# Performance work log

Hardware: AMD Instinct MI355X
Metric: run time of the kernel (lower is better)

## Reference

```python
import jax, jax.numpy as jnp
import numpy as np

ACT_BW = 8
PAR_BW = 4
EPS = 1e-8

def fake_quant(t, bw):
    # symmetric per-tensor fake quantization with dynamic absmax observer
    qmax = float(2 ** (bw - 1) - 1)
    scale = jnp.maximum(jnp.max(jnp.abs(t)) / qmax, EPS)
    q = jnp.clip(jnp.round(t / scale), -qmax, qmax) * scale
    # straight-through estimator (matches torch fake-quant backward)
    return t + jax.lax.stop_gradient(q - t)

def setup_inputs() -> dict:
    key = jax.random.key(0)
    k1, k2, k3 = jax.random.split(key, 3)
    tokens, d_in, d_out = 4096, 4096, 4096
    x = jax.random.normal(k1, (tokens, d_in), dtype=jnp.float32)
    # kaiming-uniform-ish init scale
    bound_w = 1.0 / np.sqrt(d_in)
    weight = jax.random.uniform(k2, (d_out, d_in), dtype=jnp.float32, minval=-bound_w, maxval=bound_w)
    b = jax.random.uniform(k3, (d_out,), dtype=jnp.float32, minval=-bound_w, maxval=bound_w)
    return {"x": x, "weight": weight, "b": b}

def reference(x, weight, b):
    # 1) requantize input activations (act_bitwidth)
    xq = fake_quant(x, ACT_BW)
    # 2) quantize weight (par_bitwidth), transpose [out,in] -> [in,out]
    wq = fake_quant(weight, PAR_BW).T
    # 3) quantize bias (act_bitwidth)
    bq = fake_quant(b, ACT_BW)
    # 4) AddMM: bias + x @ w^T, then requantize the output (multiplier's quantizer)
    out = bq + jnp.matmul(xq, wq)  # [tokens, out_features]
    return fake_quant(out, ACT_BW)
```

## Files before the change

kernel.cpp:

```cpp
#include <hip/hip_runtime.h>

#define NELEM (4096 * 4096)
#define KDIM 4096
#define NDIM 4096
#define DOUT 4096
#define EPSQ 1e-8f
#define STRIDE_MEM (2048 * 256)

typedef __attribute__((ext_vector_type(4))) int i32x4;
typedef __attribute__((ext_vector_type(16))) int i32x16;

typedef __attribute__((address_space(3))) void lds_void;
typedef const __attribute__((address_space(1))) void gbl_void;

__device__ __forceinline__ void load_lds16(const void* g, void* l) {
    __builtin_amdgcn_global_load_lds((gbl_void*)g, (lds_void*)l, 16, 0, 0);
}

__device__ __forceinline__ float wave_max64(float v) {
#pragma unroll
    for (int off = 32; off > 0; off >>= 1)
        v = fmaxf(v, __shfl_down(v, off));
    return v;
}


__global__ __launch_bounds__(256) void absmax_xwb(
    const float4* __restrict__ x, const float4* __restrict__ w,
    const float* __restrict__ b, unsigned* __restrict__ amax)
{
    float mx = 0.f, mw = 0.f;
    int i = blockIdx.x * 256 + threadIdx.x;
#pragma unroll
    for (int it = 0; it < 8; ++it, i += STRIDE_MEM) {
        float4 a = x[i];
        float4 c = w[i];
        mx = fmaxf(mx, fmaxf(fmaxf(fabsf(a.x), fabsf(a.y)), fmaxf(fabsf(a.z), fabsf(a.w))));
        mw = fmaxf(mw, fmaxf(fmaxf(fabsf(c.x), fabsf(c.y)), fmaxf(fabsf(c.z), fabsf(c.w))));
    }
    float mb = 0.f;
    if (blockIdx.x == 0) {
#pragma unroll
        for (int t = 0; t < DOUT / 256; ++t)
            mb = fmaxf(mb, fabsf(b[t * 256 + threadIdx.x]));
    }

    mx = wave_max64(mx); mw = wave_max64(mw); mb = wave_max64(mb);
    __shared__ float red[3][4];
    const int wave = threadIdx.x >> 6, lane = threadIdx.x & 63;
    if (lane == 0) { red[0][wave] = mx; red[1][wave] = mw; red[2][wave] = mb; }
    __syncthreads();
    if (threadIdx.x == 0) {
        float r0 = fmaxf(fmaxf(red[0][0], red[0][1]), fmaxf(red[0][2], red[0][3]));
        float r1 = fmaxf(fmaxf(red[1][0], red[1][1]), fmaxf(red[1][2], red[1][3]));
        const int sl = (blockIdx.x & 7) * 16;
        atomicMax(&amax[sl], __float_as_uint(r0));
        atomicMax(&amax[sl + 4], __float_as_uint(r1));
        if (blockIdx.x == 0) {
            float r2 = fmaxf(fmaxf(red[2][0], red[2][1]), fmaxf(red[2][2], red[2][3]));
            atomicMax(&amax[128], __float_as_uint(r2));
        }
    }
}

__device__ __forceinline__ void load_scales(const unsigned* __restrict__ amax,
                                            float& sx, float& sw) {
    float sxm = 0.f, swm = 0.f;
#pragma unroll
    for (int j = 0; j < 8; ++j) {
        sxm = fmaxf(sxm, __uint_as_float(amax[j * 16]));
        swm = fmaxf(swm, __uint_as_float(amax[j * 16 + 4]));
    }
    sx = fmaxf(sxm / 127.0f, EPSQ);
    sw = fmaxf(swm / 7.0f, EPSQ);
}

__device__ __forceinline__ int pack4(float4 a, float s, float qmax) {
    int b0 = (int)fminf(fmaxf(rintf(a.x / s), -qmax), qmax);
    int b1 = (int)fminf(fmaxf(rintf(a.y / s), -qmax), qmax);
    int b2 = (int)fminf(fmaxf(rintf(a.z / s), -qmax), qmax);
    int b3 = (int)fminf(fmaxf(rintf(a.w / s), -qmax), qmax);
    return (b0 & 0xff) | ((b1 & 0xff) << 8) | ((b2 & 0xff) << 16) | (b3 << 24);
}

__global__ __launch_bounds__(256) void quant_xwb(
    const float4* __restrict__ x, const float4* __restrict__ w,
    const float* __restrict__ b, const unsigned* __restrict__ amax,
    int* __restrict__ qx, int* __restrict__ qw, float* __restrict__ bq)
{
    float sx, sw;
    load_scales(amax, sx, sw);
    int i = blockIdx.x * 256 + threadIdx.x;
#pragma unroll
    for (int it = 0; it < 8; ++it, i += STRIDE_MEM) {
        qx[i] = pack4(x[i], sx, 127.f);
        qw[i] = pack4(w[i], sw, 7.f);
    }
    if (blockIdx.x == 0) {
        const float sb = fmaxf(__uint_as_float(amax[128]) / 127.0f, EPSQ);
#pragma unroll
        for (int t = 0; t < DOUT / 256; ++t) {
            int j = t * 256 + threadIdx.x;
            float q = fminf(fmaxf(rintf(b[j] / sb), -127.f), 127.f);
            bq[j] = q * sb;
        }
    }
}

__global__ __launch_bounds__(512, 2) void gemm_i8_8p(
    const char* __restrict__ qx,
    const char* __restrict__ qw,
    const float* __restrict__ bq,
    const unsigned* __restrict__ amax,
    float* __restrict__ out,
    unsigned* __restrict__ amax_out)
{
    constexpr int K = KDIM, N = NDIM;
    __shared__ char lds[131072];
    char* ldsA = lds;
    char* ldsB = lds + 65536;

    const int tid = threadIdx.x;
    const int wave = tid >> 6, lane = tid & 63;
    const int swz = (blockIdx.x & 7) * 32 + (blockIdx.x >> 3);
    const int bm = swz >> 4, bn = swz & 15;
    const int wm2 = wave >> 2;
    const int wn4 = wave & 3;

    const int sg16 = (((lane & 3) ^ ((lane >> 3) & 3)) << 4);
    const char* aG = qx + (size_t)(bm * 256 + wave * 16 + (lane >> 2)) * K + sg16;
    const char* bG = qw + (size_t)(bn * 256 + wave * 16 + (lane >> 2)) * K + sg16;

    const int l31 = lane & 31;
    const int fks0 = ((((lane >> 5)) ^ ((lane >> 1) & 3)) << 4);
    const int fks1 = ((((lane >> 5) | 2) ^ ((lane >> 1) & 3)) << 4);
    const int aBase = wm2 * 8192 + l31 * 64;
    const int bBase = (wn4 >> 1) * 8192 + (wn4 & 1) * 4096 + l31 * 64;

    i32x16 acc[4][2] = {};
    i32x4 XA[4], XB[2], YA[4], YB[2], A1[4], B1[2];

#define STAGE8(s) { const int p_ = (s) & 3;                                                  \
    load_lds16(aG + (size_t)(s) * 64,                   ldsA + p_ * 16384 + wave * 1024);    \
    load_lds16(aG + (size_t)128 * K + (size_t)(s) * 64, ldsA + p_ * 16384 + 8192 + wave * 1024); \
    load_lds16(bG + (size_t)(s) * 64,                   ldsB + p_ * 16384 + wave * 1024);    \
    load_lds16(bG + (size_t)128 * K + (size_t)(s) * 64, ldsB + p_ * 16384 + 8192 + wave * 1024); }

#define PHASE(s, CA, CB, NA, NB, VMN, DO_ST, DO_NXT) {                                       \
    asm volatile("s_waitcnt vmcnt(%0)" :: "n"(VMN) : "memory");                              \
    __builtin_amdgcn_s_barrier();                                                            \
    __builtin_amdgcn_sched_barrier(0);                                                       \
    if (DO_ST) STAGE8((s) + 3);                                                              \
    { const char* Ab_ = ldsA + ((s) & 3) * 16384 + aBase;                                    \
      const char* Bb_ = ldsB + ((s) & 3) * 16384 + bBase;                                    \
      _Pragma("unroll") for (int mi = 0; mi < 4; ++mi)                                       \
          A1[mi] = *(const i32x4*)(Ab_ + mi * 2048 + fks1);                                  \
      _Pragma("unroll") for (int ni = 0; ni < 2; ++ni)                                       \
          B1[ni] = *(const i32x4*)(Bb_ + ni * 2048 + fks1);                                  \
    }                                                                                        \
    __builtin_amdgcn_sched_barrier(0);                                                       \
    __builtin_amdgcn_s_setprio(1);                                                           \
    _Pragma("unroll") for (int mi = 0; mi < 4; ++mi)                                         \
    _Pragma("unroll") for (int ni = 0; ni < 2; ++ni)                                         \
        acc[mi][ni] = __builtin_amdgcn_mfma_i32_32x32x32_i8(CA[mi], CB[ni], acc[mi][ni], 0, 0, 0); \
    __builtin_amdgcn_s_setprio(0);                                                           \
    __builtin_amdgcn_sched_barrier(0);                                                       \
    if (DO_NXT) {                                                                            \
      const char* An_ = ldsA + (((s) + 1) & 3) * 16384 + aBase;                              \
      const char* Bn_ = ldsB + (((s) + 1) & 3) * 16384 + bBase;                              \
      _Pragma("unroll") for (int mi = 0; mi < 4; ++mi)                                       \
          NA[mi] = *(const i32x4*)(An_ + mi * 2048 + fks0);                                  \
      _Pragma("unroll") for (int ni = 0; ni < 2; ++ni)                                       \
          NB[ni] = *(const i32x4*)(Bn_ + ni * 2048 + fks0);                                  \
    }                                                                                        \
    __builtin_amdgcn_sched_barrier(0);                                                       \
    __builtin_amdgcn_s_setprio(1);                                                           \
    _Pragma("unroll") for (int mi = 0; mi < 4; ++mi)                                         \
    _Pragma("unroll") for (int ni = 0; ni < 2; ++ni)                                         \
        acc[mi][ni] = __builtin_amdgcn_mfma_i32_32x32x32_i8(A1[mi], B1[ni], acc[mi][ni], 0, 0, 0); \
    __builtin_amdgcn_s_setprio(0); }

    STAGE8(0); STAGE8(1); STAGE8(2);
    asm volatile("s_waitcnt vmcnt(8)" ::: "memory");
    __builtin_amdgcn_s_barrier();
    __builtin_amdgcn_sched_barrier(0);
    {
        const char* Ab_ = ldsA + aBase;
        const char* Bb_ = ldsB + bBase;
#pragma unroll
        for (int mi = 0; mi < 4; ++mi) XA[mi] = *(const i32x4*)(Ab_ + mi * 2048 + fks0);
#pragma unroll
        for (int ni = 0; ni < 2; ++ni) XB[ni] = *(const i32x4*)(Bb_ + ni * 2048 + fks0);
    }

    for (int s = 0; s < 60; s += 2) {
        PHASE(s,     XA, XB, YA, YB, 4, true, true);
        PHASE(s + 1, YA, YB, XA, XB, 4, true, true);
    }
    PHASE(60, XA, XB, YA, YB, 4, true,  true);
    PHASE(61, YA, YB, XA, XB, 4, false, true);
    PHASE(62, XA, XB, YA, YB, 0, false, true);
    PHASE(63, YA, YB, XA, XB, 0, false, false);

#undef PHASE
#undef STAGE8

    float sx, sw;
    load_scales(amax, sx, sw);
    const float s = sx * sw;
    const int col = l31;
    const int r4 = (lane >> 5) * 4;
    float am = 0.f;
    float bqv[2];
#pragma unroll
    for (int ni = 0; ni < 2; ++ni) bqv[ni] = bq[bn * 256 + wn4 * 64 + ni * 32 + col];

#pragma unroll
    for (int mi = 0; mi < 4; ++mi) {
#pragma unroll
        for (int reg = 0; reg < 16; ++reg) {
            const int row = (reg & 3) + 8 * (reg >> 2) + r4;
            const int m = bm * 256 + wm2 * 128 + mi * 32 + row;
            float* orow = out + (size_t)m * N + bn * 256 + wn4 * 64 + col;
#pragma unroll
            for (int ni = 0; ni < 2; ++ni) {
                float o = fmaf(s, (float)acc[mi][ni][reg], bqv[ni]);
                am = fmaxf(am, fabsf(o));
                orow[ni * 32] = o;
            }
        }
    }
    am = wave_max64(am);
    float* red = (float*)lds;
    if (lane == 0) red[wave] = am;
    __syncthreads();
    if (tid == 0) {
        float r = fmaxf(fmaxf(fmaxf(red[0], red[1]), fmaxf(red[2], red[3])),
                        fmaxf(fmaxf(red[4], red[5]), fmaxf(red[6], red[7])));
        atomicMax(amax_out, __float_as_uint(r));
    }
}

__global__ __launch_bounds__(256) void final_quant(
    float4* __restrict__ out, const unsigned* __restrict__ amax_out)
{
    const float so = fmaxf(__uint_as_float(amax_out[0]) / 127.0f, EPSQ);
    int i = blockIdx.x * 256 + threadIdx.x;
#pragma unroll
    for (int it = 0; it < 8; ++it, i += STRIDE_MEM) {
        float4 v = out[i];
        v.x = fminf(fmaxf(rintf(v.x / so), -127.f), 127.f) * so;
        v.y = fminf(fmaxf(rintf(v.y / so), -127.f), 127.f) * so;
        v.z = fminf(fmaxf(rintf(v.z / so), -127.f), 127.f) * so;
        v.w = fminf(fmaxf(rintf(v.w / so), -127.f), 127.f) * so;
        out[i] = v;
    }
}

extern "C" void kernel_launch(void* const* d_in, const int* in_sizes, int n_in,
                              void* d_out, int out_size, void* d_ws, size_t ws_size,
                              hipStream_t stream) {
    const float* x = (const float*)d_in[0];
    const float* w = (const float*)d_in[1];
    const float* b = (const float*)d_in[2];
    float* out = (float*)d_out;

    char* ws = (char*)d_ws;
    unsigned* amax = (unsigned*)ws;
    float* bq = (float*)(ws + 1024);
    char* qx = (char*)(ws + 32768);
    char* qw = (char*)(ws + 32768 + (size_t)NELEM);

    hipMemsetAsync(amax, 0, 1024, stream);
    hipLaunchKernelGGL(absmax_xwb, dim3(2048), dim3(256), 0, stream,
                       (const float4*)x, (const float4*)w, b, amax);
    hipLaunchKernelGGL(quant_xwb, dim3(2048), dim3(256), 0, stream,
                       (const float4*)x, (const float4*)w, b, amax,
                       (int*)qx, (int*)qw, bq);
    hipLaunchKernelGGL(gemm_i8_8p, dim3(256), dim3(512), 0, stream,
                       (const char*)qx, (const char*)qw, bq, amax, out, amax + 132);
    hipLaunchKernelGGL(final_quant, dim3(2048), dim3(256), 0, stream,
                       (float4*)out, amax + 132);
}
```

Baseline: 278.1 us.

## Fuse output requantization into GEMM epilogue via grid-wide absmax barrier

The GEMM epilogue first computes each block's output absmax and publishes it with an atomic. All blocks then spin on a completion counter until the global max is known, and each block quantizes its own outputs before storing them. This removes the separate read-modify-write pass over the 64MB output in final_quant, which now exits early when a flag shows the fused path succeeded. The spin relies on all 256 blocks being co-resident and falls back through a timeout flag. The LDS swizzle pattern is also changed to add a wave/lane XOR term, aimed at reducing bank conflicts.

```diff
diff --git a/kernel.cpp b/kernel.cpp
--- a/kernel.cpp
+++ b/kernel.cpp
@@ -113,7 +113,7 @@
     const float* __restrict__ bq,
     const unsigned* __restrict__ amax,
     float* __restrict__ out,
-    unsigned* __restrict__ amax_out)
+    unsigned* __restrict__ ws)
 {
     constexpr int K = KDIM, N = NDIM;
     __shared__ char lds[131072];
@@ -127,13 +127,14 @@
     const int wm2 = wave >> 2;
     const int wn4 = wave & 3;
 
-    const int sg16 = (((lane & 3) ^ ((lane >> 3) & 3)) << 4);
+    const int sg16 = (((lane & 3) ^ ((lane >> 3) & 3) ^ (wave & 1)) << 4);
     const char* aG = qx + (size_t)(bm * 256 + wave * 16 + (lane >> 2)) * K + sg16;
     const char* bG = qw + (size_t)(bn * 256 + wave * 16 + (lane >> 2)) * K + sg16;
 
     const int l31 = lane & 31;
-    const int fks0 = ((((lane >> 5)) ^ ((lane >> 1) & 3)) << 4);
-    const int fks1 = ((((lane >> 5) | 2) ^ ((lane >> 1) & 3)) << 4);
+    const int fx = ((lane >> 1) & 3) ^ ((lane >> 4) & 1);
+    const int fks0 = (((lane >> 5) ^ fx) << 4);
+    const int fks1 = ((((lane >> 5) | 2) ^ fx) << 4);
     const int aBase = wm2 * 8192 + l31 * 64;
     const int bBase = (wn4 >> 1) * 8192 + (wn4 & 1) * 4096 + l31 * 64;
 
@@ -216,6 +217,52 @@
     for (int ni = 0; ni < 2; ++ni) bqv[ni] = bq[bn * 256 + wn4 * 64 + ni * 32 + col];
 
 #pragma unroll
+    for (int mi = 0; mi < 4; ++mi)
+#pragma unroll
+        for (int reg = 0; reg < 16; ++reg)
+#pragma unroll
+            for (int ni = 0; ni < 2; ++ni) {
+                float o = fmaf(s, (float)acc[mi][ni][reg], bqv[ni]);
+                am = fmaxf(am, fabsf(o));
+            }
+    am = wave_max64(am);
+    float* red = (float*)lds;
+    if (lane == 0) red[wave] = am;
+    __syncthreads();
+
+    unsigned* amax_out = ws + 132;
+    unsigned* done = ws + 136;
+    unsigned* flag = ws + 140;
+    if (tid == 0) {
+        float r = fmaxf(fmaxf(fmaxf(red[0], red[1]), fmaxf(red[2], red[3])),
+                        fmaxf(fmaxf(red[4], red[5]), fmaxf(red[6], red[7])));
+        atomicMax(amax_out, __float_as_uint(r));
+        __threadfence();
+        unsigned old = atomicAdd(done, 1u);
+        float so = -1.f;
+        if (old == 255u) {
+            __threadfence();
+            atomicOr(flag, 1u);
+            so = fmaxf(__uint_as_float(atomicMax(amax_out, 0u)) / 127.0f, EPSQ);
+        } else {
+            int iters = 0;
+            while (__hip_atomic_load(done, __ATOMIC_RELAXED, __HIP_MEMORY_SCOPE_AGENT) < 256u) {
+                __builtin_amdgcn_s_sleep(2);
+                if (++iters > 150000) break;
+            }
+            if (iters > 150000) {
+                atomicOr(flag, 2u);
+            } else {
+                __threadfence();
+                so = fmaxf(__uint_as_float(atomicMax(amax_out, 0u)) / 127.0f, EPSQ);
+            }
+        }
+        red[12] = so;
+    }
+    __syncthreads();
+    const float so = red[12];
+
+#pragma unroll
     for (int mi = 0; mi < 4; ++mi) {
 #pragma unroll
         for (int reg = 0; reg < 16; ++reg) {
@@ -225,26 +272,19 @@
 #pragma unroll
             for (int ni = 0; ni < 2; ++ni) {
                 float o = fmaf(s, (float)acc[mi][ni][reg], bqv[ni]);
-                am = fmaxf(am, fabsf(o));
+                if (so > 0.f)
+                    o = fminf(fmaxf(rintf(o / so), -127.f), 127.f) * so;
                 orow[ni * 32] = o;
             }
         }
     }
-    am = wave_max64(am);
-    float* red = (float*)lds;
-    if (lane == 0) red[wave] = am;
-    __syncthreads();
-    if (tid == 0) {
-        float r = fmaxf(fmaxf(fmaxf(red[0], red[1]), fmaxf(red[2], red[3])),
-                        fmaxf(fmaxf(red[4], red[5]), fmaxf(red[6], red[7])));
-        atomicMax(amax_out, __float_as_uint(r));
-    }
 }
 
 __global__ __launch_bounds__(256) void final_quant(
-    float4* __restrict__ out, const unsigned* __restrict__ amax_out)
+    float4* __restrict__ out, const unsigned* __restrict__ ws)
 {
-    const float so = fmaxf(__uint_as_float(amax_out[0]) / 127.0f, EPSQ);
+    if (ws[140] == 1u) return;
+    const float so = fmaxf(__uint_as_float(ws[132]) / 127.0f, EPSQ);
     int i = blockIdx.x * 256 + threadIdx.x;
 #pragma unroll
     for (int it = 0; it < 8; ++it, i += STRIDE_MEM) {
@@ -278,7 +318,7 @@
                        (const float4*)x, (const float4*)w, b, amax,
                        (int*)qx, (int*)qw, bq);
     hipLaunchKernelGGL(gemm_i8_8p, dim3(256), dim3(512), 0, stream,
-                       (const char*)qx, (const char*)qw, bq, amax, out, amax + 132);
+                       (const char*)qx, (const char*)qw, bq, amax, out, amax);
     hipLaunchKernelGGL(final_quant, dim3(2048), dim3(256), 0, stream,
-                       (float4*)out, amax + 132);
-}
+                       (float4*)out, amax);
+}
```

Measured after the change: 278.6 us. About the same (+0.2%).
